# Optimization experiments

Measured on AMD Instinct MI355X. Metric: run time of the kernel, lower is better.

## Reference

```python
import jax, jax.numpy as jnp
import numpy as np

B, N, K_NB, C, KERNEL, OUT = 32, 128, 16, 1024, 8, 1024
TWO_PI = 2.0 * np.pi
EPS = 1e-14


def setup_inputs() -> dict:
    key = jax.random.key(0)
    ks = jax.random.split(key, 9)
    return {
        "node_feats": jax.random.normal(ks[0], (B, N, C), dtype=jnp.float32),
        "node_centre": jax.random.uniform(ks[1], (B, N, 2), dtype=jnp.float32),
        "neighbor_idx": jax.random.randint(ks[2], (B, N, K_NB), 0, N, dtype=jnp.int32),
        "graph_weights": jax.random.uniform(ks[3], (B, N, K_NB), dtype=jnp.float32),
        "mean_rho": jax.random.uniform(ks[4], (1, KERNEL), dtype=jnp.float32),
        "mean_theta": jax.random.uniform(ks[5], (1, KERNEL), minval=-np.pi, maxval=np.pi, dtype=jnp.float32),
        "precision_rho": jax.random.uniform(ks[6], (1, KERNEL), dtype=jnp.float32),
        "precision_theta": jax.random.uniform(ks[7], (1, KERNEL), dtype=jnp.float32),
        "conv_w": jax.random.normal(ks[8], (KERNEL, C, OUT // KERNEL), dtype=jnp.float32) * 0.02,
    }


def _gaussian_weights(node_centre, neighbor_idx, mean_rho, mean_theta, precision_rho, precision_theta):
    # gather neighbor centres per batch: [B,N,K,2]
    centre_j = jax.vmap(lambda c, idx: c[idx])(node_centre, neighbor_idx)
    diff = node_centre[:, :, None, :] - centre_j           # node_i - node_j
    cx, cy = diff[..., 0], diff[..., 1]                    # chunk order: x first
    rho = jnp.sqrt(cx ** 2 + cy ** 2)                      # [B,N,K]
    theta = jnp.arctan2(cx, cy)                            # note: atan2(x, y) as in source
    d_rho = (rho[..., None] - mean_rho[0]) ** 2            # [B,N,K,KERNEL]
    w_rho = jnp.exp(-0.5 * d_rho / (EPS + precision_rho[0] ** 2))
    a1 = jnp.abs(theta[..., None] - mean_theta[0])
    a2 = jnp.abs(TWO_PI - a1)
    w_theta = jnp.exp(-0.5 * jnp.minimum(a1, a2) ** 2 / (EPS + precision_theta[0] ** 2))
    w = w_rho * w_theta
    w = jnp.where(jnp.isnan(w), 0.0, w)
    return w / jnp.sum(w, axis=-1, keepdims=True)          # normalize over kernel dim


def reference(node_feats, node_centre, neighbor_idx, graph_weights,
              mean_rho, mean_theta, precision_rho, precision_theta, conv_w):
    gw = _gaussian_weights(node_centre, neighbor_idx, mean_rho, mean_theta,
                           precision_rho, precision_theta)       # [B,N,K,KERNEL]
    edge_w = graph_weights[..., None] * gw                        # use_graph_weights=True
    # gather neighbor features per batch: [B,N,K,C]
    feats_j = jax.vmap(lambda f, idx: f[idx])(node_feats, neighbor_idx)
    # bmm aggregation: [B,N,KERNEL,C]
    agg = jnp.einsum('bnkm,bnkc->bnmc', edge_w, feats_j)
    # per-kernel linear (no bias) then concat: [B,N,KERNEL,OUT//KERNEL] -> [B,N,OUT]
    out = jnp.einsum('bnmc,mcd->bnmd', agg, conv_w)
    out = out.reshape(node_feats.shape[0], node_feats.shape[1], -1)
    return jax.nn.relu(out)
```

## Files before the change

### kernel.cpp

```cpp
#include <hip/hip_runtime.h>
#include <hip/hip_bf16.h>

#define B_   32
#define N_   128
#define KNB  16
#define C_   1024
#define KER  8
#define DOUT 128
#define OUTC 1024
#define BN_TOT (B_ * N_)
#define BK   64
#define NT   (C_ / BK)

typedef __attribute__((ext_vector_type(8))) short bf16x8;
typedef __attribute__((ext_vector_type(4))) float f32x4;

__device__ __forceinline__ ushort f2bf(float f) {
    unsigned u = __builtin_bit_cast(unsigned, f);
    unsigned r = (u + 0x7FFFu + ((u >> 16) & 1u)) >> 16;
    return (ushort)r;
}

#define GLOAD_LDS16(gp, lp)                                                    \
    __builtin_amdgcn_global_load_lds(                                          \
        (__attribute__((address_space(1))) void*)(gp),                         \
        (__attribute__((address_space(3))) void*)(lp), 16, 0, 0)

__global__ __launch_bounds__(256) void k_prep(const float* __restrict__ f,
                                              ushort* __restrict__ Fb,
                                              const float* __restrict__ cw,
                                              ushort* __restrict__ WbT,
                                              const float* __restrict__ centre,
                                              const int* __restrict__ nidx,
                                              const float* __restrict__ gw,
                                              const float* __restrict__ mr,
                                              const float* __restrict__ mt,
                                              const float* __restrict__ pr,
                                              const float* __restrict__ pt,
                                              float* __restrict__ ew) {
    __shared__ float tile[32][33];
    int bid = blockIdx.x;
    int tid = threadIdx.x;
    if (bid < 4096) {
        int t = bid * 256 + tid;
        float4 v = ((const float4*)f)[t];
        ushort4 o;
        o.x = f2bf(v.x); o.y = f2bf(v.y); o.z = f2bf(v.z); o.w = f2bf(v.w);
        ((ushort4*)Fb)[t] = o;
    } else if (bid < 5120) {
        int b2 = bid - 4096;
        int dt = b2 & 3;
        int ct = (b2 >> 2) & 31;
        int m  = b2 >> 7;
        int tx = tid & 31;
        int ty = tid >> 5;
#pragma unroll
        for (int i = 0; i < 4; ++i) {
            int cr = ty + i * 8;
            tile[cr][tx] = cw[((size_t)m * C_ + (ct * 32 + cr)) * DOUT + dt * 32 + tx];
        }
        __syncthreads();
#pragma unroll
        for (int i = 0; i < 4; ++i) {
            int dr = ty + i * 8;
            WbT[((size_t)(m * DOUT + dt * 32 + dr)) * C_ + ct * 32 + tx] = f2bf(tile[tx][dr]);
        }
    } else {
        int t = (bid - 5120) * 256 + tid;
        int bn = t >> 4;
        int b  = bn >> 7;
        float2 ci = *(const float2*)(centre + (size_t)bn * 2);
        int j = nidx[t];
        float2 cj = *(const float2*)(centre + (size_t)(b * N_ + j) * 2);
        float cx = ci.x - cj.x, cy = ci.y - cj.y;
        float rho = sqrtf(cx * cx + cy * cy);
        float theta = atan2f(cx, cy);
        float w[KER];
        float sum = 0.f;
#pragma unroll
        for (int m = 0; m < KER; ++m) {
            float dr = rho - mr[m];
            float wr = expf(-0.5f * dr * dr / (1e-14f + pr[m] * pr[m]));
            float a1 = fabsf(theta - mt[m]);
            float a2 = fabsf(6.2831853071795864f - a1);
            float am = fminf(a1, a2);
            float wt = expf(-0.5f * am * am / (1e-14f + pt[m] * pt[m]));
            float wv = wr * wt;
            if (isnan(wv)) wv = 0.f;
            w[m] = wv;
            sum += wv;
        }
        float scale = gw[t] / sum;
#pragma unroll
        for (int m = 0; m < KER; ++m) ew[(size_t)t * KER + m] = w[m] * scale;
    }
}

__global__ __launch_bounds__(512) void k_gemm_fused(const ushort* __restrict__ Fb,
                                                    const ushort* __restrict__ WbT,
                                                    const float* __restrict__ ew,
                                                    const int* __restrict__ nidx,
                                                    float* __restrict__ out) {
    __shared__ __align__(16) char smem[98304];

    int tid  = threadIdx.x;
    int wave = tid >> 6;
    int lane = tid & 63;
    int wm = wave >> 2;
    int wn = wave & 3;
    int lr = lane & 15;
    int kg = lane >> 4;
    int b = blockIdx.x;
    int m = blockIdx.y;

    const ushort* Abase = Fb  + (size_t)b * N_ * C_;
    const ushort* Bbase = WbT + (size_t)m * DOUT * C_;

    f32x4 acc[4][2];
#pragma unroll
    for (int i = 0; i < 4; ++i)
#pragma unroll
        for (int j = 0; j < 2; ++j) acc[i][j] = (f32x4){0.f, 0.f, 0.f, 0.f};

    auto STAGE = [&](int buf, int kt) {
        ushort* As = (ushort*)(smem + buf * 32768);
        ushort* Bs = (ushort*)(smem + buf * 32768 + 16384);
#pragma unroll
        for (int i = 0; i < 2; ++i) {
            int segb = i * 512 + wave * 64;
            int seg  = segb + lane;
            int row  = seg >> 3;
            int ch   = (seg & 7) ^ (row & 7);
            const ushort* ga = Abase + (size_t)row * C_ + kt * BK + ch * 8;
            GLOAD_LDS16(ga, As + segb * 8);
            const ushort* gb = Bbase + (size_t)row * C_ + kt * BK + ch * 8;
            GLOAD_LDS16(gb, Bs + segb * 8);
        }
    };

    int aoff[4][2], boff[2][2];
#pragma unroll
    for (int mi = 0; mi < 4; ++mi)
#pragma unroll
        for (int kk = 0; kk < 2; ++kk) {
            int row = wm * 64 + mi * 16 + lr;
            int ch  = (kk * 4 + kg) ^ (row & 7);
            aoff[mi][kk] = row * 128 + ch * 16;
        }
#pragma unroll
    for (int ni = 0; ni < 2; ++ni)
#pragma unroll
        for (int kk = 0; kk < 2; ++kk) {
            int row = wn * 32 + ni * 16 + lr;
            int ch  = (kk * 4 + kg) ^ (row & 7);
            boff[ni][kk] = 16384 + row * 128 + ch * 16;
        }

    STAGE(0, 0);
    STAGE(1, 1);
    for (int kt = 0; kt < NT; ++kt) {
        int cur = kt % 3;
        const char* bufp = smem + cur * 32768;
        if (kt + 2 < NT) {
            STAGE((kt + 2) % 3, kt + 2);
            asm volatile("s_waitcnt vmcnt(8)" ::: "memory");
        } else if (kt + 1 < NT) {
            asm volatile("s_waitcnt vmcnt(4)" ::: "memory");
        } else {
            asm volatile("s_waitcnt vmcnt(0)" ::: "memory");
        }
        __builtin_amdgcn_s_barrier();
#pragma unroll
        for (int kk = 0; kk < 2; ++kk) {
            bf16x8 af[4], bv[2];
#pragma unroll
            for (int mi = 0; mi < 4; ++mi)
                af[mi] = *(const bf16x8*)(bufp + aoff[mi][kk]);
#pragma unroll
            for (int ni = 0; ni < 2; ++ni)
                bv[ni] = *(const bf16x8*)(bufp + boff[ni][kk]);
#pragma unroll
            for (int mi = 0; mi < 4; ++mi)
#pragma unroll
                for (int ni = 0; ni < 2; ++ni)
                    acc[mi][ni] = __builtin_amdgcn_mfma_f32_16x16x32_bf16(
                        af[mi], bv[ni], acc[mi][ni], 0, 0, 0);
        }
        asm volatile("" ::: "memory");
        __builtin_amdgcn_s_barrier();
    }

    float* Gt = (float*)smem;
#pragma unroll
    for (int mi = 0; mi < 4; ++mi)
#pragma unroll
        for (int ni = 0; ni < 2; ++ni)
#pragma unroll
            for (int r = 0; r < 4; ++r) {
                int grow = wm * 64 + mi * 16 + kg * 4 + r;
                int gcol = wn * 32 + ni * 16 + lr;
                Gt[grow * 132 + gcol] = acc[mi][ni][r];
            }
    __syncthreads();

    int n = tid >> 2, q = tid & 3;
    const int*   ip = nidx + (size_t)(b * N_ + n) * KNB;
    const float* ep = ew   + (size_t)(b * N_ + n) * (KNB * KER) + m;
    int rot[8];
#pragma unroll
    for (int i = 0; i < 8; ++i) rot[i] = (q * 4 + i * 4) & 31;
    f32x4 o[8];
#pragma unroll
    for (int i = 0; i < 8; ++i) o[i] = (f32x4){0.f, 0.f, 0.f, 0.f};
#pragma unroll
    for (int k = 0; k < KNB; ++k) {
        int j = ip[k];
        float w = ep[k * KER];
        const float* gr = Gt + j * 132 + q * 32;
#pragma unroll
        for (int i = 0; i < 8; ++i) {
            f32x4 v = *(const f32x4*)(gr + rot[i]);
            o[i] += v * w;
        }
    }
    float* op = out + (size_t)(b * N_ + n) * OUTC + m * DOUT + q * 32;
#pragma unroll
    for (int i = 0; i < 8; ++i) {
        f32x4 r = o[i];
#pragma unroll
        for (int jj = 0; jj < 4; ++jj) r[jj] = fmaxf(r[jj], 0.f);
        *(f32x4*)(op + rot[i]) = r;
    }
}

extern "C" void kernel_launch(void* const* d_in, const int* in_sizes, int n_in,
                              void* d_out, int out_size, void* d_ws, size_t ws_size,
                              hipStream_t stream) {
    const float* node_feats      = (const float*)d_in[0];
    const float* node_centre     = (const float*)d_in[1];
    const int*   neighbor_idx    = (const int*)d_in[2];
    const float* graph_weights   = (const float*)d_in[3];
    const float* mean_rho        = (const float*)d_in[4];
    const float* mean_theta      = (const float*)d_in[5];
    const float* precision_rho   = (const float*)d_in[6];
    const float* precision_theta = (const float*)d_in[7];
    const float* conv_w          = (const float*)d_in[8];
    float* out = (float*)d_out;

    char* ws = (char*)d_ws;
    ushort* Fb  = (ushort*)(ws);
    ushort* WbT = (ushort*)(ws + (8u  << 20));
    float*  ew  = (float*) (ws + (10u << 20));

    k_prep<<<5376, 256, 0, stream>>>(node_feats, Fb, conv_w, WbT,
                                     node_centre, neighbor_idx, graph_weights,
                                     mean_rho, mean_theta,
                                     precision_rho, precision_theta, ew);
    dim3 ggrid(B_, KER);
    k_gemm_fused<<<ggrid, 512, 0, stream>>>(Fb, WbT, ew, neighbor_idx, out);
}
```

Before: 110.1 us.

## Replace LDS-pipelined GEMM with direct-register loads and split-K across wave groups

Drops the triple-buffered LDS staging of A/B tiles. Each wave now loads its bf16 MFMA fragments straight from global memory into registers. Waves are split into two K-halves, each computing a 64x64 sub-tile, and the halves are reduced through LDS before the neighbor-gather epilogue. Neighbor indices and edge weights are prefetched before the reduction so their latency overlaps it. This removes LDS traffic and barriers from the main loop, at the cost of uncoalesced 16-byte strided global loads with no software pipelining and higher register pressure (16 accumulators per wave).

```diff
diff --git a/kernel.cpp b/kernel.cpp
--- a/kernel.cpp
+++ b/kernel.cpp
@@ -8,9 +8,6 @@
 #define KER  8
 #define DOUT 128
 #define OUTC 1024
-#define BN_TOT (B_ * N_)
-#define BK   64
-#define NT   (C_ / BK)
 
 typedef __attribute__((ext_vector_type(8))) short bf16x8;
 typedef __attribute__((ext_vector_type(4))) float f32x4;
@@ -20,11 +17,6 @@
     unsigned r = (u + 0x7FFFu + ((u >> 16) & 1u)) >> 16;
     return (ushort)r;
 }
-
-#define GLOAD_LDS16(gp, lp)                                                    \
-    __builtin_amdgcn_global_load_lds(                                          \
-        (__attribute__((address_space(1))) void*)(gp),                         \
-        (__attribute__((address_space(3))) void*)(lp), 16, 0, 0)
 
 __global__ __launch_bounds__(256) void k_prep(const float* __restrict__ f,
                                               ushort* __restrict__ Fb,
@@ -96,127 +88,100 @@
     }
 }
 
-__global__ __launch_bounds__(512) void k_gemm_fused(const ushort* __restrict__ Fb,
-                                                    const ushort* __restrict__ WbT,
-                                                    const float* __restrict__ ew,
-                                                    const int* __restrict__ nidx,
-                                                    float* __restrict__ out) {
-    __shared__ __align__(16) char smem[98304];
+__global__ __launch_bounds__(512, 2) void k_fused(const ushort* __restrict__ Fb,
+                                                  const ushort* __restrict__ WbT,
+                                                  const float* __restrict__ ew,
+                                                  const int* __restrict__ nidx,
+                                                  float* __restrict__ out) {
+    __shared__ float Gt[128 * 132];
 
     int tid  = threadIdx.x;
     int wave = tid >> 6;
     int lane = tid & 63;
-    int wm = wave >> 2;
-    int wn = wave & 3;
+    int kq = wave >> 2;
+    int rh = (wave >> 1) & 1;
+    int ch = wave & 1;
     int lr = lane & 15;
     int kg = lane >> 4;
-    int b = blockIdx.x;
-    int m = blockIdx.y;
-
-    const ushort* Abase = Fb  + (size_t)b * N_ * C_;
-    const ushort* Bbase = WbT + (size_t)m * DOUT * C_;
-
-    f32x4 acc[4][2];
+    int bid = blockIdx.x;
+    int b = bid & 31;
+    int m = bid >> 5;
+
+    const ushort* Ab = Fb  + ((size_t)(b * N_ + rh * 64 + lr)) * C_ + kq * 512 + kg * 8;
+    const ushort* Bb = WbT + ((size_t)(m * DOUT + ch * 64 + lr)) * C_ + kq * 512 + kg * 8;
+
+    f32x4 acc[4][4];
 #pragma unroll
     for (int i = 0; i < 4; ++i)
 #pragma unroll
-        for (int j = 0; j < 2; ++j) acc[i][j] = (f32x4){0.f, 0.f, 0.f, 0.f};
-
-    auto STAGE = [&](int buf, int kt) {
-        ushort* As = (ushort*)(smem + buf * 32768);
-        ushort* Bs = (ushort*)(smem + buf * 32768 + 16384);
-#pragma unroll
-        for (int i = 0; i < 2; ++i) {
-            int segb = i * 512 + wave * 64;
-            int seg  = segb + lane;
-            int row  = seg >> 3;
-            int ch   = (seg & 7) ^ (row & 7);
-            const ushort* ga = Abase + (size_t)row * C_ + kt * BK + ch * 8;
-            GLOAD_LDS16(ga, As + segb * 8);
-            const ushort* gb = Bbase + (size_t)row * C_ + kt * BK + ch * 8;
-            GLOAD_LDS16(gb, Bs + segb * 8);
-        }
-    };
-
-    int aoff[4][2], boff[2][2];
-#pragma unroll
-    for (int mi = 0; mi < 4; ++mi)
-#pragma unroll
-        for (int kk = 0; kk < 2; ++kk) {
-            int row = wm * 64 + mi * 16 + lr;
-            int ch  = (kk * 4 + kg) ^ (row & 7);
-            aoff[mi][kk] = row * 128 + ch * 16;
-        }
-#pragma unroll
-    for (int ni = 0; ni < 2; ++ni)
-#pragma unroll
-        for (int kk = 0; kk < 2; ++kk) {
-            int row = wn * 32 + ni * 16 + lr;
-            int ch  = (kk * 4 + kg) ^ (row & 7);
-            boff[ni][kk] = 16384 + row * 128 + ch * 16;
-        }
-
-    STAGE(0, 0);
-    STAGE(1, 1);
-    for (int kt = 0; kt < NT; ++kt) {
-        int cur = kt % 3;
-        const char* bufp = smem + cur * 32768;
-        if (kt + 2 < NT) {
-            STAGE((kt + 2) % 3, kt + 2);
-            asm volatile("s_waitcnt vmcnt(8)" ::: "memory");
-        } else if (kt + 1 < NT) {
-            asm volatile("s_waitcnt vmcnt(4)" ::: "memory");
-        } else {
-            asm volatile("s_waitcnt vmcnt(0)" ::: "memory");
-        }
-        __builtin_amdgcn_s_barrier();
-#pragma unroll
-        for (int kk = 0; kk < 2; ++kk) {
-            bf16x8 af[4], bv[2];
-#pragma unroll
-            for (int mi = 0; mi < 4; ++mi)
-                af[mi] = *(const bf16x8*)(bufp + aoff[mi][kk]);
-#pragma unroll
-            for (int ni = 0; ni < 2; ++ni)
-                bv[ni] = *(const bf16x8*)(bufp + boff[ni][kk]);
-#pragma unroll
-            for (int mi = 0; mi < 4; ++mi)
-#pragma unroll
-                for (int ni = 0; ni < 2; ++ni)
-                    acc[mi][ni] = __builtin_amdgcn_mfma_f32_16x16x32_bf16(
-                        af[mi], bv[ni], acc[mi][ni], 0, 0, 0);
-        }
-        asm volatile("" ::: "memory");
-        __builtin_amdgcn_s_barrier();
-    }
-
-    float* Gt = (float*)smem;
-#pragma unroll
-    for (int mi = 0; mi < 4; ++mi)
-#pragma unroll
-        for (int ni = 0; ni < 2; ++ni)
-#pragma unroll
-            for (int r = 0; r < 4; ++r) {
-                int grow = wm * 64 + mi * 16 + kg * 4 + r;
-                int gcol = wn * 32 + ni * 16 + lr;
-                Gt[grow * 132 + gcol] = acc[mi][ni][r];
-            }
+        for (int j = 0; j < 4; ++j) acc[i][j] = (f32x4){0.f, 0.f, 0.f, 0.f};
+
+#pragma unroll
+    for (int s = 0; s < 16; ++s) {
+        bf16x8 av[4], bv[4];
+#pragma unroll
+        for (int i = 0; i < 4; ++i) {
+            av[i] = *(const bf16x8*)(Ab + (size_t)i * 16 * C_ + s * 32);
+            bv[i] = *(const bf16x8*)(Bb + (size_t)i * 16 * C_ + s * 32);
+        }
+#pragma unroll
+        for (int mi = 0; mi < 4; ++mi)
+#pragma unroll
+            for (int nj = 0; nj < 4; ++nj)
+                acc[mi][nj] = __builtin_amdgcn_mfma_f32_16x16x32_bf16(
+                    av[mi], bv[nj], acc[mi][nj], 0, 0, 0);
+    }
+
+    int n = tid >> 2, q = tid & 3;
+    const int* ip = nidx + (size_t)(b * N_ + n) * KNB;
+    int4 jv0 = *(const int4*)(ip);
+    int4 jv1 = *(const int4*)(ip + 4);
+    int4 jv2 = *(const int4*)(ip + 8);
+    int4 jv3 = *(const int4*)(ip + 12);
+    const float* ep = ew + (size_t)(b * N_ + n) * (KNB * KER) + m;
+    float wv[KNB];
+#pragma unroll
+    for (int k = 0; k < KNB; ++k) wv[k] = ep[k * KER];
+
+    if (kq == 0) {
+#pragma unroll
+        for (int mi = 0; mi < 4; ++mi)
+#pragma unroll
+            for (int nj = 0; nj < 4; ++nj)
+#pragma unroll
+                for (int r = 0; r < 4; ++r) {
+                    int grow = rh * 64 + mi * 16 + kg * 4 + r;
+                    int gcol = ch * 64 + nj * 16 + lr;
+                    Gt[grow * 132 + gcol] = acc[mi][nj][r];
+                }
+    }
     __syncthreads();
-
-    int n = tid >> 2, q = tid & 3;
-    const int*   ip = nidx + (size_t)(b * N_ + n) * KNB;
-    const float* ep = ew   + (size_t)(b * N_ + n) * (KNB * KER) + m;
+    if (kq == 1) {
+#pragma unroll
+        for (int mi = 0; mi < 4; ++mi)
+#pragma unroll
+            for (int nj = 0; nj < 4; ++nj)
+#pragma unroll
+                for (int r = 0; r < 4; ++r) {
+                    int grow = rh * 64 + mi * 16 + kg * 4 + r;
+                    int gcol = ch * 64 + nj * 16 + lr;
+                    Gt[grow * 132 + gcol] += acc[mi][nj][r];
+                }
+    }
+    __syncthreads();
+
     int rot[8];
 #pragma unroll
     for (int i = 0; i < 8; ++i) rot[i] = (q * 4 + i * 4) & 31;
     f32x4 o[8];
 #pragma unroll
     for (int i = 0; i < 8; ++i) o[i] = (f32x4){0.f, 0.f, 0.f, 0.f};
+    int jarr[KNB] = {jv0.x, jv0.y, jv0.z, jv0.w, jv1.x, jv1.y, jv1.z, jv1.w,
+                     jv2.x, jv2.y, jv2.z, jv2.w, jv3.x, jv3.y, jv3.z, jv3.w};
 #pragma unroll
     for (int k = 0; k < KNB; ++k) {
-        int j = ip[k];
-        float w = ep[k * KER];
-        const float* gr = Gt + j * 132 + q * 32;
+        const float* gr = Gt + jarr[k] * 132 + q * 32;
+        float w = wv[k];
 #pragma unroll
         for (int i = 0; i < 8; ++i) {
             f32x4 v = *(const f32x4*)(gr + rot[i]);
@@ -256,6 +221,5 @@
                                      node_centre, neighbor_idx, graph_weights,
                                      mean_rho, mean_theta,
                                      precision_rho, precision_theta, ew);
-    dim3 ggrid(B_, KER);
-    k_gemm_fused<<<ggrid, 512, 0, stream>>>(Fb, WbT, ew, neighbor_idx, out);
-}
+    k_fused<<<256, 512, 0, stream>>>(Fb, WbT, ew, neighbor_idx, out);
+}
```

New measurement: 130.8 us. 1.19x slower.
